# Kernel tuning notes

Hardware: AMD Instinct MI355X
Metric: run time of the kernel (lower is better)

## Reference

```python
import math
import jax, jax.numpy as jnp
import numpy as np

B, T, C, H = 2, 2048, 1024, 16
D = C // H


def _slopes(n):
    def p2(m):
        start = 2 ** (-(2 ** -(math.log2(m) - 3)))
        return [start * start ** i for i in range(m)]
    if math.log2(n).is_integer():
        return p2(n)
    c = 2 ** math.floor(math.log2(n))
    return p2(c) + _slopes(2 * c)[0::2][: n - c]


def setup_inputs() -> dict:
    key = jax.random.key(0)
    ks = jax.random.split(key, 9)
    std = 0.02
    x = jax.random.normal(ks[0], (B, T, C), dtype=jnp.float32)
    Wq = std * jax.random.normal(ks[1], (C, C), dtype=jnp.float32)
    Wk = std * jax.random.normal(ks[2], (C, C), dtype=jnp.float32)
    Wv = std * jax.random.normal(ks[3], (C, C), dtype=jnp.float32)
    # fc_resid init: std 0.02/sqrt(num_layers)
    Wo = (std / math.sqrt(24.0)) * jax.random.normal(ks[4], (C, C), dtype=jnp.float32)
    bq = jnp.zeros((C,), jnp.float32)
    bk = jnp.zeros((C,), jnp.float32)
    bv = jnp.zeros((C,), jnp.float32)
    bo = jnp.zeros((C,), jnp.float32)
    return {"x": x, "Wq": Wq, "bq": bq, "Wk": Wk, "bk": bk,
            "Wv": Wv, "bv": bv, "Wo": Wo, "bo": bo}


def reference(x, Wq, bq, Wk, bk, Wv, bv, Wo, bo):
    # projections -> [B, T, H, D]
    q = (x @ Wq + bq).reshape(B, T, H, D)
    k = (x @ Wk + bk).reshape(B, T, H, D)
    v = (x @ Wv + bv).reshape(B, T, H, D)

    scale = 1.0 / math.sqrt(D)
    att = jnp.einsum("bqhd,bkhd->bhqk", q, k) * scale  # [B,H,T,T]

    slopes = jnp.asarray(_slopes(H), dtype=jnp.float32)  # [H]
    i = jnp.arange(T)
    rel = i[None, :] - i[None, :].T  # rel[i,j] = j - i
    causal = rel <= 0  # j <= i
    # alibi bias: -tril(i - j) = tril(j - i), scaled per head
    alibi = slopes[:, None, None] * jnp.where(causal, rel, 0).astype(jnp.float32)

    att = att + alibi[None]  # broadcast over batch
    att = jnp.where(causal[None, None], att, -jnp.inf)
    att = jax.nn.softmax(att, axis=-1)

    y = jnp.einsum("bhqk,bkhd->bqhd", att, v).reshape(B, T, C)
    return y @ Wo + bo  # dropout p=0 (eval) is identity
```

## Files before the change

### kernel.cpp

```cpp
#include <hip/hip_runtime.h>
#include <hip/hip_bf16.h>

typedef __bf16 bf16;
typedef __bf16 bf16x4 __attribute__((ext_vector_type(4)));
typedef __bf16 bf16x8 __attribute__((ext_vector_type(8)));
typedef float floatx4 __attribute__((ext_vector_type(4)));

#define B_ 2
#define T_ 2048
#define C_ 1024
#define H_ 16
#define D_ 64
#define M_ 4096
#define QK_LD 2048

__device__ __forceinline__ void load_lds16(const void* g, void* l) {
  __builtin_amdgcn_global_load_lds(
      (const __attribute__((address_space(1))) unsigned int*)g,
      (__attribute__((address_space(3))) unsigned int*)l, 16, 0, 0);
}

struct PrepArgs { const float* w[4]; bf16* wt[4]; const float* x; bf16* xb; };

__global__ __launch_bounds__(256)
void prep(PrepArgs p) {
  const int bid = blockIdx.x;
  if (bid < 4096) {
    __shared__ float tile[32][33];
    const int z = bid >> 10, xy = bid & 1023;
    const int bx = xy & 31, by = xy >> 5;
    const float* in = p.w[z];
    bf16* out = p.wt[z];
    int tx = threadIdx.x & 31, ty = threadIdx.x >> 5;
    int n0 = bx * 32, k0 = by * 32;
#pragma unroll
    for (int j = 0; j < 32; j += 8)
      tile[ty + j][tx] = in[(size_t)(k0 + ty + j) * C_ + n0 + tx];
    __syncthreads();
#pragma unroll
    for (int j = 0; j < 32; j += 8)
      out[(size_t)(n0 + ty + j) * C_ + k0 + tx] = (bf16)tile[tx][ty + j];
  } else {
    int i = ((bid - 4096) * 256 + threadIdx.x) * 8;
    float4 a = *(const float4*)(p.x + i);
    float4 b = *(const float4*)(p.x + i + 4);
    bf16x8 o;
    o[0] = (bf16)a.x; o[1] = (bf16)a.y; o[2] = (bf16)a.z; o[3] = (bf16)a.w;
    o[4] = (bf16)b.x; o[5] = (bf16)b.y; o[6] = (bf16)b.z; o[7] = (bf16)b.w;
    *(bf16x8*)(p.xb + i) = o;
  }
}

struct GQ {
  const bf16* A; const bf16* Bt;
  const float* bias[3];
  bf16* Cout; bf16* vt; int N; int K;
};

__global__ __launch_bounds__(256, 2)
void gemm128(GQ g) {
  __shared__ __align__(16) bf16 As[128 * 64];
  __shared__ __align__(16) bf16 Bs[128 * 64];
  const int tid = threadIdx.x;
  const int wave = tid >> 6, lane = tid & 63;
  const int quad = lane >> 4, l16 = lane & 15;
  const int m0 = blockIdx.y * 128, n0 = blockIdx.x * 128;
  const int wm = (wave >> 1) * 64, wn = (wave & 1) * 64;

  floatx4 acc[4][4] = {};

  int rA[4], cA[4];
#pragma unroll
  for (int t = 0; t < 4; ++t) {
    int pch = (wave * 4 + t) * 64 + lane;
    rA[t] = pch >> 3;
    cA[t] = (pch & 7) ^ (rA[t] & 7);
  }

  for (int k0 = 0; k0 < g.K; k0 += 64) {
    __syncthreads();
#pragma unroll
    for (int t = 0; t < 4; ++t) {
      load_lds16(g.A + (size_t)(m0 + rA[t]) * g.K + k0 + cA[t] * 8,
                 As + (wave * 4 + t) * 512);
      load_lds16(g.Bt + (size_t)(n0 + rA[t]) * g.K + k0 + cA[t] * 8,
                 Bs + (wave * 4 + t) * 512);
    }
    __builtin_amdgcn_s_waitcnt(0x0f70);
    __syncthreads();
#pragma unroll
    for (int s = 0; s < 2; ++s) {
      bf16x8 af[4], bfr[4];
#pragma unroll
      for (int i = 0; i < 4; ++i) {
        int mr = wm + i * 16 + l16;
        af[i] = *(const bf16x8*)(As + ((mr * 8) + ((s * 4 + quad) ^ (mr & 7))) * 8);
        int nr = wn + i * 16 + l16;
        bfr[i] = *(const bf16x8*)(Bs + ((nr * 8) + ((s * 4 + quad) ^ (nr & 7))) * 8);
      }
#pragma unroll
      for (int i = 0; i < 4; ++i)
#pragma unroll
        for (int j = 0; j < 4; ++j)
          acc[i][j] = __builtin_amdgcn_mfma_f32_16x16x32_bf16(af[i], bfr[j],
                                                              acc[i][j], 0, 0, 0);
    }
  }

  const bool vsplit = (n0 >= 2048);
#pragma unroll
  for (int j = 0; j < 4; ++j) {
    int col = n0 + wn + j * 16 + l16;
    const float* bp = g.bias[col >> 10];
    float bv = bp[col & 1023];
    if (vsplit) {
      int cv = col - 2048;
      bf16* dst0 = g.vt + ((size_t)((m0 >> 11) * 16 + (cv >> 6)) * 64 + (cv & 63)) * (size_t)T_
                   + (m0 & 2047) + wm + quad * 4;
#pragma unroll
      for (int i = 0; i < 4; ++i) {
        bf16x4 pk;
#pragma unroll
        for (int r = 0; r < 4; ++r) pk[r] = (bf16)(acc[i][j][r] + bv);
        *(bf16x4*)(dst0 + i * 16) = pk;
      }
    } else {
#pragma unroll
      for (int i = 0; i < 4; ++i) {
#pragma unroll
        for (int r = 0; r < 4; ++r) {
          int row = m0 + wm + i * 16 + quad * 4 + r;
          g.Cout[(size_t)row * g.N + col] = (bf16)(acc[i][j][r] + bv);
        }
      }
    }
  }
}

__global__ __launch_bounds__(256, 2)
void gemm_out(const bf16* __restrict__ A, const bf16* __restrict__ Bt,
              const float* __restrict__ bias, float* __restrict__ C) {
  __shared__ __align__(16) bf16 As[64 * 64];
  __shared__ __align__(16) bf16 Bs[128 * 64];
  const int tid = threadIdx.x;
  const int wave = tid >> 6, lane = tid & 63;
  const int quad = lane >> 4, l16 = lane & 15;
  const int m0 = blockIdx.y * 64, n0 = blockIdx.x * 128;
  const int wm = (wave >> 1) * 32, wn = (wave & 1) * 64;

  floatx4 acc[2][4] = {};

  int rA[2], cA[2], rB[4], cB[4];
#pragma unroll
  for (int t = 0; t < 2; ++t) {
    int p = t * 256 + tid;
    rA[t] = p >> 3; cA[t] = (p & 7) ^ (rA[t] & 7);
  }
#pragma unroll
  for (int t = 0; t < 4; ++t) {
    int p = t * 256 + tid;
    rB[t] = p >> 3; cB[t] = (p & 7) ^ (rB[t] & 7);
  }

  for (int k0 = 0; k0 < 1024; k0 += 64) {
    __syncthreads();
#pragma unroll
    for (int t = 0; t < 2; ++t)
      load_lds16(A + (size_t)(m0 + rA[t]) * 1024 + k0 + cA[t] * 8,
                 As + t * 2048 + wave * 512);
#pragma unroll
    for (int t = 0; t < 4; ++t)
      load_lds16(Bt + (size_t)(n0 + rB[t]) * 1024 + k0 + cB[t] * 8,
                 Bs + t * 2048 + wave * 512);
    __builtin_amdgcn_s_waitcnt(0x0f70);
    __syncthreads();
#pragma unroll
    for (int s = 0; s < 2; ++s) {
      bf16x8 af[2], bfr[4];
#pragma unroll
      for (int i = 0; i < 2; ++i) {
        int mr = wm + i * 16 + l16;
        af[i] = *(const bf16x8*)(As + ((mr * 8) + ((s * 4 + quad) ^ (mr & 7))) * 8);
      }
#pragma unroll
      for (int j = 0; j < 4; ++j) {
        int nr = wn + j * 16 + l16;
        bfr[j] = *(const bf16x8*)(Bs + ((nr * 8) + ((s * 4 + quad) ^ (nr & 7))) * 8);
      }
#pragma unroll
      for (int i = 0; i < 2; ++i)
#pragma unroll
        for (int j = 0; j < 4; ++j)
          acc[i][j] = __builtin_amdgcn_mfma_f32_16x16x32_bf16(af[i], bfr[j],
                                                              acc[i][j], 0, 0, 0);
    }
  }

#pragma unroll
  for (int j = 0; j < 4; ++j) {
    int col = n0 + wn + j * 16 + l16;
    float bv = bias[col];
#pragma unroll
    for (int i = 0; i < 2; ++i)
#pragma unroll
      for (int r = 0; r < 4; ++r) {
        int row = m0 + wm + i * 16 + quad * 4 + r;
        C[(size_t)row * 1024 + col] = acc[i][j][r] + bv;
      }
  }
}

__global__ __launch_bounds__(256, 2)
void attn8(const bf16* __restrict__ qk, const bf16* __restrict__ vt,
           bf16* __restrict__ y, bf16* __restrict__ po, float* __restrict__ pl) {
  __shared__ __align__(16) bf16 Kl[2][64 * 64];
  __shared__ __align__(16) bf16 Vl[2][64 * 64];
  __shared__ __align__(16) bf16 Pl[4][16 * 68];
  const int tid = threadIdx.x, wave = tid >> 6, lane = tid & 63;
  const int quad = lane >> 4, l16 = lane & 15;
  const int bh = blockIdx.x, b = bh >> 4, h = bh & 15;
  const int yy = blockIdx.y;
  int qb, kbeg, kcnt, seg;
  if (yy < 8)       { qb = yy;      kbeg = 0;      kcnt = 2 * qb + 2; seg = -1; }
  else if (yy < 16) { qb = 23 - yy; kbeg = 0;      kcnt = qb + 1;     seg = 0;  }
  else              { qb = 31 - yy; kbeg = qb + 1; kcnt = qb + 1;     seg = 1;  }

  const float L2E = 1.4426950408889634f;
  const float slope2 = exp2f(-0.5f * (float)(h + 1)) * L2E;
  const float scl2 = 0.125f * L2E;
  const float M0 = 14.0f;

  bf16x8 ones;
  {
    bf16 v1 = (l16 == 0) ? (bf16)1.0f : (bf16)0.0f;
#pragma unroll
    for (int j = 0; j < 8; ++j) ones[j] = v1;
  }

  int rS[2], cS[2];
#pragma unroll
  for (int t = 0; t < 2; ++t) {
    int p = t * 256 + tid;
    rS[t] = p >> 3;
    cS[t] = (p & 7) ^ (rS[t] & 7);
  }
  const bf16* kbase = qk + (size_t)b * T_ * QK_LD + 1024 + h * 64;
  const bf16* vbase = vt + (size_t)bh * 64 * T_;

  bf16* Plw = Pl[wave];
  const int q0 = qb * 128;
  const int w0 = q0 + wave * 32;

  bf16x8 qf[2][2];
  float rowoff[2][4];
#pragma unroll
  for (int qt = 0; qt < 2; ++qt) {
#pragma unroll
    for (int s = 0; s < 2; ++s)
      qf[qt][s] = *(const bf16x8*)(qk +
          (size_t)(b * T_ + w0 + qt * 16 + l16) * QK_LD + h * 64 + s * 32 + quad * 8);
#pragma unroll
    for (int r = 0; r < 4; ++r)
      rowoff[qt][r] = slope2 * (float)(w0 + qt * 16 + quad * 4 + r) + M0;
  }

  floatx4 o[2][5];
#pragma unroll
  for (int qt = 0; qt < 2; ++qt)
#pragma unroll
    for (int n = 0; n < 5; ++n) o[qt][n] = (floatx4)0.f;

#pragma unroll
  for (int t = 0; t < 2; ++t) {
    load_lds16(kbase + (size_t)(kbeg * 64 + rS[t]) * QK_LD + cS[t] * 8,
               Kl[0] + (t * 4 + wave) * 512);
    load_lds16(vbase + (size_t)rS[t] * T_ + kbeg * 64 + cS[t] * 8,
               Vl[0] + (t * 4 + wave) * 512);
  }
  __builtin_amdgcn_s_waitcnt(0x0f70);
  __syncthreads();

  for (int it = 0; it < kcnt; ++it) {
    const int kj0 = (kbeg + it) * 64;
    const int cur = it & 1;

    if (it + 1 < kcnt) {
      const int nk = kj0 + 64;
#pragma unroll
      for (int t = 0; t < 2; ++t) {
        load_lds16(kbase + (size_t)(nk + rS[t]) * QK_LD + cS[t] * 8,
                   Kl[cur ^ 1] + (t * 4 + wave) * 512);
        load_lds16(vbase + (size_t)rS[t] * T_ + nk + cS[t] * 8,
                   Vl[cur ^ 1] + (t * 4 + wave) * 512);
      }
    }

    const bf16* Klc = Kl[cur];
    const bf16* Vlc = Vl[cur];
    bf16x8 kf[2][4], vf[2][4];
#pragma unroll
    for (int ss = 0; ss < 2; ++ss)
#pragma unroll
      for (int kt = 0; kt < 4; ++kt) {
        const int krow = kt * 16 + l16;
        kf[ss][kt] = *(const bf16x8*)(Klc + krow * 64 + (((ss * 4 + quad) ^ (krow & 7)) * 8));
        vf[ss][kt] = *(const bf16x8*)(Vlc + krow * 64 + (((ss * 4 + quad) ^ (krow & 7)) * 8));
      }

    float scol[4];
#pragma unroll
    for (int kt = 0; kt < 4; ++kt)
      scol[kt] = slope2 * (float)(kj0 + kt * 16 + l16);

#pragma unroll
    for (int qt = 0; qt < 2; ++qt) {
      const int rb = w0 + qt * 16;
      floatx4 sa[4] = {};
#pragma unroll
      for (int ss = 0; ss < 2; ++ss)
#pragma unroll
        for (int kt = 0; kt < 4; ++kt)
          sa[kt] = __builtin_amdgcn_mfma_f32_16x16x32_bf16(qf[qt][ss], kf[ss][kt],
                                                           sa[kt], 0, 0, 0);

      if (kj0 + 63 > rb) {
#pragma unroll
        for (int kt = 0; kt < 4; ++kt)
#pragma unroll
          for (int r = 0; r < 4; ++r) {
            const int row = rb + quad * 4 + r;
            float p = __builtin_amdgcn_exp2f(
                fmaf(sa[kt][r], scl2, scol[kt]) - rowoff[qt][r]);
            if (kj0 + kt * 16 + l16 > row) p = 0.f;
            Plw[(quad * 4 + r) * 68 + kt * 16 + l16] = (bf16)p;
          }
      } else {
#pragma unroll
        for (int kt = 0; kt < 4; ++kt)
#pragma unroll
          for (int r = 0; r < 4; ++r)
            Plw[(quad * 4 + r) * 68 + kt * 16 + l16] = (bf16)__builtin_amdgcn_exp2f(
                fmaf(sa[kt][r], scl2, scol[kt]) - rowoff[qt][r]);
      }

      __builtin_amdgcn_s_waitcnt(0xc07f);

#pragma unroll
      for (int half = 0; half < 2; ++half) {
        bf16x8 pf = *(const bf16x8*)(Plw + l16 * 68 + half * 32 + quad * 8);
#pragma unroll
        for (int nt = 0; nt < 4; ++nt)
          o[qt][nt] = __builtin_amdgcn_mfma_f32_16x16x32_bf16(pf, vf[half][nt],
                                                              o[qt][nt], 0, 0, 0);
        o[qt][4] = __builtin_amdgcn_mfma_f32_16x16x32_bf16(pf, ones, o[qt][4], 0, 0, 0);
      }
    }

    __builtin_amdgcn_s_waitcnt(0x0f70);
    __syncthreads();
  }

  if (seg < 0) {
#pragma unroll
    for (int qt = 0; qt < 2; ++qt)
#pragma unroll
      for (int r = 0; r < 4; ++r) {
        float lsum = __shfl(o[qt][4][r], lane & 48);
        float inv = 1.f / lsum;
        const int row = w0 + qt * 16 + quad * 4 + r;
#pragma unroll
        for (int nt = 0; nt < 4; ++nt)
          y[(size_t)(b * T_ + row) * C_ + h * 64 + nt * 16 + l16] =
              (bf16)(o[qt][nt][r] * inv);
      }
  } else {
    const int pid = (bh * 8 + (qb - 8)) * 2 + seg;
    bf16* pob = po + (size_t)pid * 8192;
#pragma unroll
    for (int qt = 0; qt < 2; ++qt) {
#pragma unroll
      for (int half = 0; half < 2; ++half) {
        bf16x8 pk;
#pragma unroll
        for (int jj = 0; jj < 8; ++jj) {
          int j = half * 8 + jj;
          pk[jj] = (bf16)o[qt][j >> 2][j & 3];
        }
        *(bf16x8*)(pob + (qt * 2 + half) * 2048 + tid * 8) = pk;
      }
#pragma unroll
      for (int r = 0; r < 4; ++r)
        if (l16 == 0)
          pl[pid * 128 + wave * 32 + qt * 16 + quad * 4 + r] = o[qt][4][r];
    }
  }
}

__global__ __launch_bounds__(256)
void combine(const bf16* __restrict__ po, const float* __restrict__ pl,
             bf16* __restrict__ y) {
  const int x = blockIdx.x;
  const int bh = x >> 3, qb = (x & 7) + 8;
  const int b = bh >> 4, h = bh & 15;
  const int pid0 = (bh * 8 + (qb - 8)) * 2;
  const bf16* p0 = po + (size_t)pid0 * 8192;
  const bf16* p1 = p0 + 8192;
  const int t = threadIdx.x;
  const int wave = t >> 6, quad = (t >> 4) & 3, l16 = t & 15;

  float linv[2][4];
#pragma unroll
  for (int qt = 0; qt < 2; ++qt)
#pragma unroll
    for (int r = 0; r < 4; ++r) {
      const int row = wave * 32 + qt * 16 + quad * 4 + r;
      linv[qt][r] = 1.f / (pl[pid0 * 128 + row] + pl[(pid0 + 1) * 128 + row]);
    }

#pragma unroll
  for (int qt = 0; qt < 2; ++qt)
#pragma unroll
    for (int half = 0; half < 2; ++half) {
      bf16x8 a = *(const bf16x8*)(p0 + (qt * 2 + half) * 2048 + t * 8);
      bf16x8 c = *(const bf16x8*)(p1 + (qt * 2 + half) * 2048 + t * 8);
#pragma unroll
      for (int jj = 0; jj < 8; ++jj) {
        int j = half * 8 + jj;
        const int nt = j >> 2, r = j & 3;
        const int row = wave * 32 + qt * 16 + quad * 4 + r;
        const int col = nt * 16 + l16;
        float v = ((float)a[jj] + (float)c[jj]) * linv[qt][r];
        y[(size_t)(b * T_ + qb * 128 + row) * C_ + h * 64 + col] = (bf16)v;
      }
    }
}

extern "C" void kernel_launch(void* const* d_in, const int* in_sizes, int n_in,
                              void* d_out, int out_size, void* d_ws, size_t ws_size,
                              hipStream_t stream) {
  const float* x  = (const float*)d_in[0];
  const float* Wq = (const float*)d_in[1];
  const float* bq = (const float*)d_in[2];
  const float* Wk = (const float*)d_in[3];
  const float* bk = (const float*)d_in[4];
  const float* Wv = (const float*)d_in[5];
  const float* bv = (const float*)d_in[6];
  const float* Wo = (const float*)d_in[7];
  const float* bo = (const float*)d_in[8];

  bf16* ws  = (bf16*)d_ws;
  bf16* WtQ = ws;
  bf16* WtK = WtQ + (size_t)C_ * C_;
  bf16* WtV = WtK + (size_t)C_ * C_;
  bf16* WtO = WtV + (size_t)C_ * C_;
  bf16* xb  = WtO + (size_t)C_ * C_;
  bf16* qkb = xb + (size_t)M_ * C_;
  bf16* vtb = qkb + (size_t)M_ * 2 * C_;
  bf16* yb  = vtb + (size_t)M_ * C_;
  bf16* pob = yb + (size_t)M_ * C_;
  float* plb = (float*)(pob + (size_t)512 * 8192);

  PrepArgs pp;
  pp.w[0] = Wq; pp.w[1] = Wk; pp.w[2] = Wv; pp.w[3] = Wo;
  pp.wt[0] = WtQ; pp.wt[1] = WtK; pp.wt[2] = WtV; pp.wt[3] = WtO;
  pp.x = x; pp.xb = xb;
  prep<<<dim3(4096 + M_ * C_ / (256 * 8)), 256, 0, stream>>>(pp);

  GQ gq;
  gq.A = xb; gq.Bt = WtQ;
  gq.bias[0] = bq; gq.bias[1] = bk; gq.bias[2] = bv;
  gq.Cout = qkb; gq.vt = vtb; gq.N = 2 * C_; gq.K = C_;
  gemm128<<<dim3(24, 32), 256, 0, stream>>>(gq);

  attn8<<<dim3(32, 24), 256, 0, stream>>>(qkb, vtb, yb, pob, plb);
  combine<<<dim3(32 * 8), 256, 0, stream>>>(pob, plb, yb);

  gemm_out<<<dim3(8, 64), 256, 0, stream>>>(yb, WtO, bo, (float*)d_out);
}
```

Baseline: 186.7 us.

## Split attention key tiles across wave pairs and reorder block scheduling

The attention kernel goes from 4 to 8 waves per block. Each pair of waves shares a 32-row query slice and splits every 64-key tile into two 32-key halves, and the partial outputs and row sums are reduced through LDS at the end. A constant table also remaps blockIdx.y so that long and short query blocks are interleaved for better load balance. This is meant to raise parallelism and shorten the per-block critical path, at the cost of an extra LDS reduction, a barrier, and more register pressure under the 512-thread launch bound.

```diff
diff --git a/kernel.cpp b/kernel.cpp
--- a/kernel.cpp
+++ b/kernel.cpp
@@ -210,16 +210,18 @@
   }
 }
 
-__global__ __launch_bounds__(256, 2)
+__constant__ int yy_map[24] = {7, 8, 16, 9, 17, 6, 10, 18, 11, 19, 5, 12,
+                               20, 13, 21, 4, 14, 22, 15, 23, 3, 2, 1, 0};
+
+__global__ __launch_bounds__(512, 4)
 void attn8(const bf16* __restrict__ qk, const bf16* __restrict__ vt,
            bf16* __restrict__ y, bf16* __restrict__ po, float* __restrict__ pl) {
-  __shared__ __align__(16) bf16 Kl[2][64 * 64];
-  __shared__ __align__(16) bf16 Vl[2][64 * 64];
-  __shared__ __align__(16) bf16 Pl[4][16 * 68];
+  __shared__ __align__(16) bf16 smem[8192 + 8192 + 8 * 576];
   const int tid = threadIdx.x, wave = tid >> 6, lane = tid & 63;
   const int quad = lane >> 4, l16 = lane & 15;
+  const int qs = wave >> 1, kh = wave & 1;
   const int bh = blockIdx.x, b = bh >> 4, h = bh & 15;
-  const int yy = blockIdx.y;
+  const int yy = yy_map[blockIdx.y];
   int qb, kbeg, kcnt, seg;
   if (yy < 8)       { qb = yy;      kbeg = 0;      kcnt = 2 * qb + 2; seg = -1; }
   else if (yy < 16) { qb = 23 - yy; kbeg = 0;      kcnt = qb + 1;     seg = 0;  }
@@ -237,19 +239,14 @@
     for (int j = 0; j < 8; ++j) ones[j] = v1;
   }
 
-  int rS[2], cS[2];
-#pragma unroll
-  for (int t = 0; t < 2; ++t) {
-    int p = t * 256 + tid;
-    rS[t] = p >> 3;
-    cS[t] = (p & 7) ^ (rS[t] & 7);
-  }
+  const int rS = tid >> 3;
+  const int cS = (tid & 7) ^ (rS & 7);
   const bf16* kbase = qk + (size_t)b * T_ * QK_LD + 1024 + h * 64;
   const bf16* vbase = vt + (size_t)bh * 64 * T_;
 
-  bf16* Plw = Pl[wave];
+  bf16* Plw = smem + 16384 + wave * 576;
   const int q0 = qb * 128;
-  const int w0 = q0 + wave * 32;
+  const int w0 = q0 + qs * 32;
 
   bf16x8 qf[2][2];
   float rowoff[2][4];
@@ -270,13 +267,8 @@
 #pragma unroll
     for (int n = 0; n < 5; ++n) o[qt][n] = (floatx4)0.f;
 
-#pragma unroll
-  for (int t = 0; t < 2; ++t) {
-    load_lds16(kbase + (size_t)(kbeg * 64 + rS[t]) * QK_LD + cS[t] * 8,
-               Kl[0] + (t * 4 + wave) * 512);
-    load_lds16(vbase + (size_t)rS[t] * T_ + kbeg * 64 + cS[t] * 8,
-               Vl[0] + (t * 4 + wave) * 512);
-  }
+  load_lds16(kbase + (size_t)(kbeg * 64 + rS) * QK_LD + cS * 8, smem + wave * 512);
+  load_lds16(vbase + (size_t)rS * T_ + kbeg * 64 + cS * 8, smem + 8192 + wave * 512);
   __builtin_amdgcn_s_waitcnt(0x0f70);
   __syncthreads();
 
@@ -286,79 +278,95 @@
 
     if (it + 1 < kcnt) {
       const int nk = kj0 + 64;
-#pragma unroll
-      for (int t = 0; t < 2; ++t) {
-        load_lds16(kbase + (size_t)(nk + rS[t]) * QK_LD + cS[t] * 8,
-                   Kl[cur ^ 1] + (t * 4 + wave) * 512);
-        load_lds16(vbase + (size_t)rS[t] * T_ + nk + cS[t] * 8,
-                   Vl[cur ^ 1] + (t * 4 + wave) * 512);
-      }
-    }
-
-    const bf16* Klc = Kl[cur];
-    const bf16* Vlc = Vl[cur];
-    bf16x8 kf[2][4], vf[2][4];
+      load_lds16(kbase + (size_t)(nk + rS) * QK_LD + cS * 8,
+                 smem + (cur ^ 1) * 4096 + wave * 512);
+      load_lds16(vbase + (size_t)rS * T_ + nk + cS * 8,
+                 smem + 8192 + (cur ^ 1) * 4096 + wave * 512);
+    }
+
+    const bf16* Klc = smem + cur * 4096;
+    const bf16* Vlc = smem + 8192 + cur * 4096;
+    bf16x8 kf[2][2], vf[4];
 #pragma unroll
     for (int ss = 0; ss < 2; ++ss)
 #pragma unroll
-      for (int kt = 0; kt < 4; ++kt) {
-        const int krow = kt * 16 + l16;
-        kf[ss][kt] = *(const bf16x8*)(Klc + krow * 64 + (((ss * 4 + quad) ^ (krow & 7)) * 8));
-        vf[ss][kt] = *(const bf16x8*)(Vlc + krow * 64 + (((ss * 4 + quad) ^ (krow & 7)) * 8));
-      }
-
-    float scol[4];
-#pragma unroll
-    for (int kt = 0; kt < 4; ++kt)
-      scol[kt] = slope2 * (float)(kj0 + kt * 16 + l16);
+      for (int kt = 0; kt < 2; ++kt) {
+        const int krow = kh * 32 + kt * 16 + l16;
+        kf[ss][kt] = *(const bf16x8*)(Klc + krow * 64 +
+                                      (((ss * 4 + quad) ^ (krow & 7)) * 8));
+      }
+#pragma unroll
+    for (int nt = 0; nt < 4; ++nt) {
+      const int drow = nt * 16 + l16;
+      vf[nt] = *(const bf16x8*)(Vlc + drow * 64 +
+                                (((kh * 4 + quad) ^ (drow & 7)) * 8));
+    }
+
+    float scol[2];
+#pragma unroll
+    for (int kt = 0; kt < 2; ++kt)
+      scol[kt] = slope2 * (float)(kj0 + kh * 32 + kt * 16 + l16);
 
 #pragma unroll
     for (int qt = 0; qt < 2; ++qt) {
       const int rb = w0 + qt * 16;
-      floatx4 sa[4] = {};
+      floatx4 sa[2] = {};
 #pragma unroll
       for (int ss = 0; ss < 2; ++ss)
 #pragma unroll
-        for (int kt = 0; kt < 4; ++kt)
+        for (int kt = 0; kt < 2; ++kt)
           sa[kt] = __builtin_amdgcn_mfma_f32_16x16x32_bf16(qf[qt][ss], kf[ss][kt],
                                                            sa[kt], 0, 0, 0);
 
-      if (kj0 + 63 > rb) {
-#pragma unroll
-        for (int kt = 0; kt < 4; ++kt)
+      if (kj0 + kh * 32 + 31 > rb) {
+#pragma unroll
+        for (int kt = 0; kt < 2; ++kt)
 #pragma unroll
           for (int r = 0; r < 4; ++r) {
             const int row = rb + quad * 4 + r;
             float p = __builtin_amdgcn_exp2f(
                 fmaf(sa[kt][r], scl2, scol[kt]) - rowoff[qt][r]);
-            if (kj0 + kt * 16 + l16 > row) p = 0.f;
-            Plw[(quad * 4 + r) * 68 + kt * 16 + l16] = (bf16)p;
+            if (kj0 + kh * 32 + kt * 16 + l16 > row) p = 0.f;
+            Plw[(quad * 4 + r) * 36 + kt * 16 + l16] = (bf16)p;
           }
       } else {
 #pragma unroll
-        for (int kt = 0; kt < 4; ++kt)
+        for (int kt = 0; kt < 2; ++kt)
 #pragma unroll
           for (int r = 0; r < 4; ++r)
-            Plw[(quad * 4 + r) * 68 + kt * 16 + l16] = (bf16)__builtin_amdgcn_exp2f(
+            Plw[(quad * 4 + r) * 36 + kt * 16 + l16] = (bf16)__builtin_amdgcn_exp2f(
                 fmaf(sa[kt][r], scl2, scol[kt]) - rowoff[qt][r]);
       }
 
       __builtin_amdgcn_s_waitcnt(0xc07f);
 
-#pragma unroll
-      for (int half = 0; half < 2; ++half) {
-        bf16x8 pf = *(const bf16x8*)(Plw + l16 * 68 + half * 32 + quad * 8);
-#pragma unroll
-        for (int nt = 0; nt < 4; ++nt)
-          o[qt][nt] = __builtin_amdgcn_mfma_f32_16x16x32_bf16(pf, vf[half][nt],
-                                                              o[qt][nt], 0, 0, 0);
-        o[qt][4] = __builtin_amdgcn_mfma_f32_16x16x32_bf16(pf, ones, o[qt][4], 0, 0, 0);
-      }
+      bf16x8 pf = *(const bf16x8*)(Plw + l16 * 36 + quad * 8);
+#pragma unroll
+      for (int nt = 0; nt < 4; ++nt)
+        o[qt][nt] = __builtin_amdgcn_mfma_f32_16x16x32_bf16(pf, vf[nt],
+                                                            o[qt][nt], 0, 0, 0);
+      o[qt][4] = __builtin_amdgcn_mfma_f32_16x16x32_bf16(pf, ones, o[qt][4], 0, 0, 0);
     }
 
     __builtin_amdgcn_s_waitcnt(0x0f70);
     __syncthreads();
   }
+
+  float* Cb = (float*)smem;
+  if (kh == 1) {
+#pragma unroll
+    for (int qt = 0; qt < 2; ++qt)
+#pragma unroll
+      for (int n = 0; n < 5; ++n)
+        *(floatx4*)(Cb + (((qs * 2 + qt) * 5 + n) * 64 + lane) * 4) = o[qt][n];
+  }
+  __syncthreads();
+  if (kh == 1) return;
+#pragma unroll
+  for (int qt = 0; qt < 2; ++qt)
+#pragma unroll
+    for (int n = 0; n < 5; ++n)
+      o[qt][n] += *(const floatx4*)(Cb + (((qs * 2 + qt) * 5 + n) * 64 + lane) * 4);
 
   if (seg < 0) {
 #pragma unroll
@@ -386,12 +394,12 @@
           int j = half * 8 + jj;
           pk[jj] = (bf16)o[qt][j >> 2][j & 3];
         }
-        *(bf16x8*)(pob + (qt * 2 + half) * 2048 + tid * 8) = pk;
+        *(bf16x8*)(pob + (qt * 2 + half) * 2048 + (qs * 64 + lane) * 8) = pk;
       }
 #pragma unroll
       for (int r = 0; r < 4; ++r)
         if (l16 == 0)
-          pl[pid * 128 + wave * 32 + qt * 16 + quad * 4 + r] = o[qt][4][r];
+          pl[pid * 128 + qs * 32 + qt * 16 + quad * 4 + r] = o[qt][4][r];
     }
   }
 }
@@ -472,7 +480,7 @@
   gq.Cout = qkb; gq.vt = vtb; gq.N = 2 * C_; gq.K = C_;
   gemm128<<<dim3(24, 32), 256, 0, stream>>>(gq);
 
-  attn8<<<dim3(32, 24), 256, 0, stream>>>(qkb, vtb, yb, pob, plb);
+  attn8<<<dim3(32, 24), 512, 0, stream>>>(qkb, vtb, yb, pob, plb);
   combine<<<dim3(32 * 8), 256, 0, stream>>>(pob, plb, yb);
 
   gemm_out<<<dim3(8, 64), 256, 0, stream>>>(yb, WtO, bo, (float*)d_out);
```

New measurement: 212.5 us. 1.14x slower.
